# Performance work log

Measured on AMD Instinct MI355X. Metric: run time of the kernel, lower is better.

## Reference

```python
import jax, jax.numpy as jnp
import numpy as np

# dims (see shape_source): seq S = d_t+1 must equal d_k for the unary quantum loader
B, T, D_IN = 128, 127, 48
DK = 128
S = T + 1            # tokens incl. class token; S == DK
H, L = 8, 6
P = (S * S - S) // 2  # RBS angles per head (pyramid circuit over S wires)


def _pyramid_pairs(n):
    # deterministic pyramid ordering of n(n-1)/2 adjacent-pair Givens rotations
    a, b = [], []
    for k in range(n - 1):
        for i in range(k, -1, -1):
            a.append(i)
            b.append(i + 1)
    return np.asarray(a, np.int32), np.asarray(b, np.int32)


def _build_W(phi, pa, pb, n):
    # classical simulation of the RBS pyramid circuit restricted to the unary
    # subspace: product of Givens rotations -> orthogonal n x n matrix
    def step(W, inp):
        ia, ib, th = inp
        c, s = jnp.cos(th), jnp.sin(th)
        ra, rb = W[ia], W[ib]
        W = W.at[ia].set(c * ra - s * rb)
        W = W.at[ib].set(s * ra + c * rb)
        return W, None
    W0 = jnp.eye(n, dtype=phi.dtype)
    W, _ = jax.lax.scan(step, W0, (pa, pb, phi))
    return W


def _layer_norm(x, g, b, eps=1e-5):
    m = jnp.mean(x, axis=-1, keepdims=True)
    v = jnp.mean((x - m) ** 2, axis=-1, keepdims=True)
    return (x - m) * jax.lax.rsqrt(v + eps) * g + b


def setup_inputs() -> dict:
    key = jax.random.key(0)
    ks = jax.random.split(key, 8)
    f32 = jnp.float32
    return {
        "x": jax.random.normal(ks[0], (B, T, D_IN), f32),
        "embed_w": jax.random.normal(ks[1], (DK, D_IN), f32) / np.sqrt(D_IN),
        "embed_b": jnp.zeros((DK,), f32),
        "class_token": jax.random.normal(ks[2], (DK,), f32) / DK,
        "norm0_g": jnp.ones((DK,), f32),
        "norm0_b": jnp.zeros((DK,), f32),
        "Vw": jax.random.normal(ks[3], (L, H, DK, DK), f32) / np.sqrt(DK),
        "Vb": jnp.zeros((L, H, DK), f32),
        "ln_g": jnp.ones((L, H, DK), f32),
        "ln_b": jnp.zeros((L, H, DK), f32),
        "phi": jax.random.normal(ks[4], (L, H, P), f32) / np.sqrt(S),
        "merger_w": jax.random.normal(ks[5], (L, H), f32) / np.sqrt(H),
        "merger_b": jnp.zeros((L,), f32),
    }


def reference(x, embed_w, embed_b, class_token, norm0_g, norm0_b,
              Vw, Vb, ln_g, ln_b, phi, merger_w, merger_b):
    Bsz = x.shape[0]
    pa, pb = _pyramid_pairs(S)
    # orthogonal score matrices for every (layer, head)
    Ws = jax.vmap(lambda p: _build_W(p, pa, pb, S))(phi.reshape(L * H, P))
    Ws = Ws.reshape(L, H, S, S)

    # embed patches, prepend class token (pos_embedding add is a no-op in the
    # original source: bare `+self.pos_embedding` statement, so it is omitted)
    tok = jnp.einsum('btf,df->btd', x, embed_w) + embed_b
    h = jnp.concatenate([jnp.broadcast_to(class_token, (Bsz, 1, DK)), tok], axis=1)
    h = _layer_norm(h, norm0_g, norm0_b)

    scale = 1.0 / np.sqrt(DK)
    for l in range(L):
        nrm = jnp.sqrt(jnp.sum(h * h, axis=-1))      # input3: token norms [B,S]
        u = h / nrm[..., None]                        # unit tokens (convert_array)
        hh, nn, uu = h, nrm, u

        def head(W, vw, vb, g, be):
            V = jnp.einsum('bsd,ed->bse', hh, vw) + vb
            M = jnp.einsum('bsd,de,bte->bst', uu, W, uu)
            A = (M * M) * (nn[:, :, None] * nn[:, None, :])
            Pm = jax.nn.softmax(A * scale, axis=-1)
            return _layer_norm(jnp.einsum('bst,btd->bsd', Pm, V) + hh, g, be)

        hs = jax.vmap(head)(Ws[l], Vw[l], Vb[l], ln_g[l], ln_b[l])  # [H,B,S,D]
        h = jnp.einsum('hbsd,h->bsd', hs, merger_w[l]) + merger_b[l]
    return h[:, -1, :]
```

## Files before the change

kernel.cpp:

```cpp
#include <hip/hip_runtime.h>
#include <hip/hip_bf16.h>


typedef __bf16 bf16x8 __attribute__((ext_vector_type(8)));
typedef float  f32x4  __attribute__((ext_vector_type(4)));
typedef unsigned int u32;
typedef u32 u32x4 __attribute__((ext_vector_type(4)));

__device__ __forceinline__ int sidx(int row, int col)
{
    return row * 128 + ((((col >> 3) ^ (row & 15)) << 3) | (col & 7));
}

__device__ __forceinline__ void gll16(const void* g, void* l)
{
    __builtin_amdgcn_global_load_lds(
        (const __attribute__((address_space(1))) void*)g,
        (__attribute__((address_space(3))) void*)l, 16, 0, 0);
}

__global__ void __launch_bounds__(256)
prep_kernel(const float* __restrict__ phi, float2* __restrict__ csn,
            const float* __restrict__ vw,  __bf16* __restrict__ cvwf)
{
    if (blockIdx.x < 3072) {
        const int mat = blockIdx.x >> 6;
        const int t   = ((blockIdx.x & 63) << 2) + (threadIdx.x >> 6);
        const int j   = threadIdx.x & 63;
        float th = 0.f;
        if (t < 253) {
            const int p = t & 1, i = 2 * j + p;
            const int lim = min(t, 252 - t);
            if (i <= lim) {
                const int k = (t + i) >> 1;
                th = phi[mat * 8128 + ((k * (k + 1)) >> 1) + (k - i)];
            }
        }
        float sn, cs;
        __sincosf(th, &sn, &cs);
        csn[(mat * 256 + t) * 64 + j] = make_float2(cs, sn);
    } else {
        const int f    = (blockIdx.x - 3072) * 256 + threadIdx.x;
        const int lane = f & 63;
        const int k0   = (f >> 6) & 3;
        const int t    = (f >> 8) & 7;
        const int lh   = f >> 11;
        const int row  = t * 16 + (lane & 15);
        const int col  = k0 * 32 + (lane >> 4) * 8;
        const float* src = vw + (lh * 128 + row) * 128 + col;
        __bf16* dst = cvwf + f * 8;
#pragma unroll
        for (int j2 = 0; j2 < 8; j2++) dst[j2] = (__bf16)src[j2];
    }
}

__global__ void __launch_bounds__(64)
build_w_kernel(const float2* __restrict__ csn, __bf16* __restrict__ wt)
{
    const int mat = blockIdx.x >> 5;
    const int grp = blockIdx.x & 31;
    const int c0  = grp * 4;
    const int lam = threadIdx.x;

    const float2* base = csn + (mat * 256) * 64 + lam;

    float vlo[4], vhi[4];
#pragma unroll
    for (int j = 0; j < 4; j++) {
        vlo[j] = (2 * lam     == c0 + j) ? 1.f : 0.f;
        vhi[j] = (2 * lam + 1 == c0 + j) ? 1.f : 0.f;
    }

    float2 buf[3][16];
#pragma unroll
    for (int k = 0; k < 16; k++) buf[0][k] = base[k * 64];
#pragma unroll
    for (int k = 0; k < 16; k++) buf[1][k] = base[(16 + k) * 64];

#pragma unroll
    for (int g = 0; g < 16; g++) {
        const int cb = g % 3;
        if (g < 14) {
            const int nb = (g + 2) % 3;
#pragma unroll
            for (int k = 0; k < 16; k++)
                buf[nb][k] = base[((g + 2) * 16 + k) * 64];
        }
#pragma unroll
        for (int p = 0; p < 8; p++) {
            {
                const float cs = buf[cb][2 * p].x, sn = buf[cb][2 * p].y;
#pragma unroll
                for (int j = 0; j < 4; j++) {
                    float lo = vlo[j], hi = vhi[j];
                    vlo[j] = cs * lo - sn * hi;
                    vhi[j] = sn * lo + cs * hi;
                }
            }
            {
                const float cs = buf[cb][2 * p + 1].x, sn = buf[cb][2 * p + 1].y;
#pragma unroll
                for (int j = 0; j < 4; j++) {
                    float y  = __shfl_down(vlo[j], 1);
                    float x  = vhi[j];
                    float xn = cs * x - sn * y;
                    float yn = sn * x + cs * y;
                    vhi[j] = xn;
                    float z = __shfl_up(yn, 1);
                    if (lam > 0) vlo[j] = z;
                }
            }
        }
    }

    const int t    = c0 >> 4;
    const int k0w  = lam >> 4;
    const int quad = (lam >> 2) & 3;
    u32* wtu = (u32*)wt;
#pragma unroll
    for (int j = 0; j < 4; j++) {
        __bf16 va = (__bf16)vlo[j];
        __bf16 vb = (__bf16)vhi[j];
        u32 pk = (u32)__builtin_bit_cast(unsigned short, va)
               | ((u32)__builtin_bit_cast(unsigned short, vb) << 16);
        const int frag = (t * 4 + k0w) * 64 + quad * 16 + ((c0 & 15) + j);
        wtu[mat * 8192 + frag * 4 + (lam & 3)] = pk;
    }
}

__global__ void __launch_bounds__(512)
embed_kernel(const float* __restrict__ x,  const float* __restrict__ ew,
             const float* __restrict__ eb, const float* __restrict__ ct,
             const float* __restrict__ g0, const float* __restrict__ b0,
             float* __restrict__ hf, __bf16* __restrict__ hb,
             float* __restrict__ invn)
{
    __shared__ float sx[4][48];
    __shared__ float sred[4][2];
    const int d  = threadIdx.x & 127, sq = threadIdx.x >> 7;
    const int wh = (threadIdx.x >> 6) & 1;
    const int b  = blockIdx.x & 127;
    const int s  = (blockIdx.x >> 7) * 4 + sq;

    if (s > 0 && d < 48) sx[sq][d] = x[(b * 127 + (s - 1)) * 48 + d];
    __syncthreads();

    float val;
    if (s == 0) {
        val = ct[d];
    } else {
        float aa = 0.f;
#pragma unroll
        for (int f = 0; f < 48; f++) aa = fmaf(sx[sq][f], ew[d * 48 + f], aa);
        val = aa + eb[d];
    }
    float v = val;
#pragma unroll
    for (int m = 32; m; m >>= 1) v += __shfl_xor(v, m);
    if ((threadIdx.x & 63) == 0) sred[sq][wh] = v;
    __syncthreads();
    float mean = (sred[sq][0] + sred[sq][1]) * (1.f / 128.f);
    float xc   = val - mean;
    __syncthreads();
    v = xc * xc;
#pragma unroll
    for (int m = 32; m; m >>= 1) v += __shfl_xor(v, m);
    if ((threadIdx.x & 63) == 0) sred[sq][wh] = v;
    __syncthreads();
    float var = (sred[sq][0] + sred[sq][1]) * (1.f / 128.f);
    float y   = xc * rsqrtf(var + 1e-5f) * g0[d] + b0[d];
    __syncthreads();
    v = y * y;
#pragma unroll
    for (int m = 32; m; m >>= 1) v += __shfl_xor(v, m);
    if ((threadIdx.x & 63) == 0) sred[sq][wh] = v;
    __syncthreads();
    float ss = sred[sq][0] + sred[sq][1];

    const int o = (b * 128 + s) * 128 + d;
    hf[o] = y;
    hb[o] = (__bf16)y;
    if (d == 0) invn[b * 128 + s] = rsqrtf(ss);
}

__global__ void __launch_bounds__(512, 2)
attn_kernel(int l, int last,
            const float*  __restrict__ hf,  const __bf16* __restrict__ hb,
            const float*  __restrict__ invn, const __bf16* __restrict__ wt,
            const __bf16* __restrict__ vwf, const float* __restrict__ vb,
            const float* __restrict__ lng,  const float* __restrict__ lnb,
            const float* __restrict__ mwp,  __bf16* __restrict__ hs)
{
    __shared__ __align__(16) __bf16 sH[128 * 128];
    __shared__ __align__(16) __bf16 sY[128 * 128];
    __shared__ float sInv[128];
    __shared__ float sVb[128];
    __shared__ float sLg[128];
    __shared__ float sLb[128];

    const int tid  = threadIdx.x;
    const int lane = tid & 63, w = tid >> 6;
    const int l15  = lane & 15, quad = lane >> 4;
    const int b    = blockIdx.x & 127;
    const int hh   = blockIdx.x >> 7;
    const int lh   = l * 8 + hh;

    const __bf16* hbp   = hb  + b * 16384;
    const __bf16* wbase = wt  + (size_t)lh * 16384;
    const __bf16* vbase = vwf + (size_t)lh * 16384;

#pragma unroll
    for (int c = 0; c < 4; c++) {
        const int ch  = tid + c * 512;
        const int row = ch >> 4, cc = ch & 15;
        const int sc  = cc ^ (row & 15);
        gll16(hbp + (row * 16 + sc) * 8, &sH[(c * 512 + w * 64) * 8]);
    }
    if (tid < 128) {
        sInv[tid] = invn[b * 128 + tid];
        sVb[tid]  = vb[lh * 128 + tid];
        sLg[tid]  = lng[lh * 128 + tid];
        sLb[tid]  = lnb[lh * 128 + tid];
    }
    __syncthreads();

    const int r0 = w * 16;
    const int kq = quad * 8;
    const int q4 = quad * 4;
    const f32x4 vzero = {0.f, 0.f, 0.f, 0.f};
    const bool active = !last || (w == 7);

    f32x4 acc[8];

    auto mmGA = [&](const __bf16* gB) {
#pragma unroll
        for (int t = 0; t < 8; t++) acc[t] = vzero;
        __builtin_amdgcn_s_setprio(1);
#pragma unroll
        for (int k0c = 0; k0c < 4; k0c++) {
            bf16x8 a0 = *(const bf16x8*)(&sH[sidx(r0 + l15, k0c * 32 + kq)]);
#pragma unroll
            for (int t = 0; t < 8; t++) {
                bf16x8 bb = *(const bf16x8*)(gB + ((t * 4 + k0c) * 64 + lane) * 8);
                acc[t] = __builtin_amdgcn_mfma_f32_16x16x32_bf16(a0, bb, acc[t], 0, 0, 0);
            }
        }
        __builtin_amdgcn_s_setprio(0);
    };

    auto mmLL = [&](const __bf16* Ab, const __bf16* Bb) {
#pragma unroll
        for (int t = 0; t < 8; t++) acc[t] = vzero;
        __builtin_amdgcn_s_setprio(1);
#pragma unroll
        for (int k0 = 0; k0 < 128; k0 += 32) {
            const int kk = k0 + kq;
            bf16x8 a0 = *(const bf16x8*)(&Ab[sidx(r0 + l15, kk)]);
#pragma unroll
            for (int t = 0; t < 8; t++) {
                bf16x8 bb = *(const bf16x8*)(&Bb[sidx(t * 16 + l15, kk)]);
                acc[t] = __builtin_amdgcn_mfma_f32_16x16x32_bf16(a0, bb, acc[t], 0, 0, 0);
            }
        }
        __builtin_amdgcn_s_setprio(0);
    };

    float hres[8][4];

    if (active) {
        mmGA(wbase);
#pragma unroll
        for (int t = 0; t < 8; t++)
#pragma unroll
            for (int r = 0; r < 4; r++)
                sY[sidx(r0 + q4 + r, t * 16 + l15)] = (__bf16)acc[t][r];

        mmLL(sY, sH);

        {
            const float scale2 = 0.08838834764831843f * 1.4426950408889634f;
            float invt[8];
#pragma unroll
            for (int t = 0; t < 8; t++) invt[t] = sInv[t * 16 + l15];
            float invs[4];
#pragma unroll
            for (int r = 0; r < 4; r++) invs[r] = sInv[r0 + q4 + r];

            float mx[4] = {-3e38f, -3e38f, -3e38f, -3e38f};
#pragma unroll
            for (int t = 0; t < 8; t++)
#pragma unroll
                for (int r = 0; r < 4; r++) {
                    float g = acc[t][r];
                    float v = g * g * invs[r] * invt[t] * scale2;
                    acc[t][r] = v;
                    mx[r] = fmaxf(mx[r], v);
                }
#pragma unroll
            for (int m = 1; m < 16; m <<= 1)
#pragma unroll
                for (int r = 0; r < 4; r++) mx[r] = fmaxf(mx[r], __shfl_xor(mx[r], m));

            float sm[4] = {0.f, 0.f, 0.f, 0.f};
#pragma unroll
            for (int t = 0; t < 8; t++)
#pragma unroll
                for (int r = 0; r < 4; r++) {
                    float e = exp2f(acc[t][r] - mx[r]);
                    acc[t][r] = e;
                    sm[r] += e;
                }
#pragma unroll
            for (int m = 1; m < 16; m <<= 1)
#pragma unroll
                for (int r = 0; r < 4; r++) sm[r] += __shfl_xor(sm[r], m);
#pragma unroll
            for (int r = 0; r < 4; r++) sm[r] = 1.0f / sm[r];
#pragma unroll
            for (int t = 0; t < 8; t++)
#pragma unroll
                for (int r = 0; r < 4; r++)
                    sY[sidx(r0 + q4 + r, t * 16 + l15)] = (__bf16)(acc[t][r] * sm[r]);
        }

        {
            const float* hfp = hf + (b * 128 + r0 + q4) * 128;
#pragma unroll
            for (int t = 0; t < 8; t++)
#pragma unroll
                for (int r = 0; r < 4; r++)
                    hres[t][r] = hfp[r * 128 + t * 16 + l15];
        }
    }

    mmGA(vbase);
    __syncthreads();

    {
        float vbv[8];
#pragma unroll
        for (int t = 0; t < 8; t++) vbv[t] = sVb[t * 16 + l15];
#pragma unroll
        for (int t = 0; t < 8; t++)
#pragma unroll
            for (int r = 0; r < 4; r++)
                sH[sidx(t * 16 + l15, r0 + q4 + r)] = (__bf16)(acc[t][r] + vbv[t]);
    }
    __syncthreads();

    if (active) {
        mmLL(sY, sH);

        {
            const float mw = mwp[lh];
            float lgv[8], lbv[8];
#pragma unroll
            for (int t = 0; t < 8; t++) {
                lgv[t] = sLg[t * 16 + l15];
                lbv[t] = sLb[t * 16 + l15];
            }
            float sum_[4] = {0.f, 0.f, 0.f, 0.f};
            float sq_[4]  = {0.f, 0.f, 0.f, 0.f};
#pragma unroll
            for (int t = 0; t < 8; t++)
#pragma unroll
                for (int r = 0; r < 4; r++) {
                    float xx = acc[t][r] + hres[t][r];
                    acc[t][r] = xx;
                    sum_[r] += xx;
                    sq_[r]  += xx * xx;
                }
#pragma unroll
            for (int m = 1; m < 16; m <<= 1)
#pragma unroll
                for (int r = 0; r < 4; r++) {
                    sum_[r] += __shfl_xor(sum_[r], m);
                    sq_[r]  += __shfl_xor(sq_[r], m);
                }
            float mean[4], rstd[4];
#pragma unroll
            for (int r = 0; r < 4; r++) {
                mean[r] = sum_[r] * (1.f / 128.f);
                float var = sq_[r] * (1.f / 128.f) - mean[r] * mean[r];
                rstd[r] = rsqrtf(fmaxf(var, 0.f) + 1e-5f);
            }
            __bf16* hsp = hs + ((hh * 128 + b) * 128 + r0 + q4) * 128;
#pragma unroll
            for (int t = 0; t < 8; t++)
#pragma unroll
                for (int r = 0; r < 4; r++) {
                    if (!last || (q4 + r == 15)) {
                        float y = (acc[t][r] - mean[r]) * rstd[r] * lgv[t] + lbv[t];
                        hsp[r * 128 + t * 16 + l15] = (__bf16)(y * mw);
                    }
                }
        }
    }
}

__global__ void __launch_bounds__(256)
merge_kernel(const __bf16* __restrict__ hs, const float* __restrict__ mbp, int l,
             float* __restrict__ hf, __bf16* __restrict__ hb, float* __restrict__ invn,
             float* __restrict__ out, int last)
{
    const int lane = threadIdx.x & 63;
    const int wv   = threadIdx.x >> 6;
    const int sq   = lane >> 4;
    const int dl   = lane & 15;
    const int d0   = dl * 8;
    const float mbv = mbp[l];

    int b, s;
    if (last) {
        b = blockIdx.x * 16 + wv * 4 + sq;
        s = 127;
    } else {
        b = blockIdx.x & 127;
        s = (blockIdx.x >> 7) * 16 + wv * 4 + sq;
    }

    float a[8];
#pragma unroll
    for (int j = 0; j < 8; j++) a[j] = mbv;
#pragma unroll
    for (int h8 = 0; h8 < 8; h8++) {
        bf16x8 v = *(const bf16x8*)(hs + (((size_t)h8 * 128 + b) * 128 + s) * 128 + d0);
#pragma unroll
        for (int j = 0; j < 8; j++) a[j] += (float)v[j];
    }

    if (last) {
        float4 f0 = {a[0], a[1], a[2], a[3]};
        float4 f1 = {a[4], a[5], a[6], a[7]};
        *(float4*)(out + b * 128 + d0)     = f0;
        *(float4*)(out + b * 128 + d0 + 4) = f1;
        return;
    }

    float ss = 0.f;
#pragma unroll
    for (int j = 0; j < 8; j++) ss = fmaf(a[j], a[j], ss);
#pragma unroll
    for (int m = 1; m < 16; m <<= 1) ss += __shfl_xor(ss, m);

    const size_t o = ((size_t)b * 128 + s) * 128 + d0;
    float4 f0 = {a[0], a[1], a[2], a[3]};
    float4 f1 = {a[4], a[5], a[6], a[7]};
    *(float4*)(hf + o)     = f0;
    *(float4*)(hf + o + 4) = f1;

    u32 pk[4];
#pragma unroll
    for (int j2 = 0; j2 < 4; j2++) {
        __bf16 x0 = (__bf16)a[2 * j2], x1 = (__bf16)a[2 * j2 + 1];
        pk[j2] = (u32)__builtin_bit_cast(unsigned short, x0)
               | ((u32)__builtin_bit_cast(unsigned short, x1) << 16);
    }
    u32x4 pv = {pk[0], pk[1], pk[2], pk[3]};
    *(u32x4*)(hb + o) = pv;

    if (dl == 0) invn[b * 128 + s] = rsqrtf(ss);
}

extern "C" void kernel_launch(void* const* d_in, const int* in_sizes, int n_in,
                              void* d_out, int out_size, void* d_ws, size_t ws_size,
                              hipStream_t stream)
{
    (void)in_sizes; (void)n_in; (void)out_size; (void)ws_size;

    const float* x   = (const float*)d_in[0];
    const float* ew  = (const float*)d_in[1];
    const float* eb  = (const float*)d_in[2];
    const float* ct  = (const float*)d_in[3];
    const float* g0  = (const float*)d_in[4];
    const float* b0  = (const float*)d_in[5];
    const float* vw  = (const float*)d_in[6];
    const float* vb  = (const float*)d_in[7];
    const float* lng = (const float*)d_in[8];
    const float* lnb = (const float*)d_in[9];
    const float* phi = (const float*)d_in[10];
    const float* mw  = (const float*)d_in[11];
    const float* mb  = (const float*)d_in[12];
    float* out = (float*)d_out;

    char* ws = (char*)d_ws;
    __bf16* wt   = (__bf16*)(ws);
    float*  hf   = (float*)(ws + 1572864);
    __bf16* hb   = (__bf16*)(ws + 9961472);
    float*  invn = (float*)(ws + 14155776);
    __bf16* hs   = (__bf16*)(ws + 14221312);
    __bf16* cvwf = (__bf16*)(ws + 47775744);
    float2* csn  = (float2*)(ws + 49348608);

    prep_kernel<<<3456, 256, 0, stream>>>(phi, csn, vw, cvwf);
    build_w_kernel<<<1536, 64, 0, stream>>>(csn, wt);
    embed_kernel<<<4096, 512, 0, stream>>>(x, ew, eb, ct, g0, b0, hf, hb, invn);
    for (int l = 0; l < 6; l++) {
        const int last = (l == 5) ? 1 : 0;
        attn_kernel<<<1024, 512, 0, stream>>>(l, last, hf, hb, invn, wt, cvwf,
                                              vb, lng, lnb, mw, hs);
        merge_kernel<<<last ? 8 : 1024, 256, 0, stream>>>(hs, mb, l, hf, hb,
                                                          invn, out, last);
    }
}
```

Before: 412.7 us.

## Process two heads per attention block and pre-sum their outputs

Each attention block now handles two heads (hp and hp+4) one after the other. The first head's layernormed, merger-weighted result is kept packed in registers as bf16 and added to the second head's result before storing. This halves the grid and the bytes written to the hs buffer, and the merge kernel reads only 4 head slices instead of 8. The cost is fewer blocks for occupancy, a reload of sH between heads, extra registers, and an extra bf16 rounding in the partial sum.

```diff
diff --git a/kernel.cpp b/kernel.cpp
--- a/kernel.cpp
+++ b/kernel.cpp
@@ -6,6 +6,7 @@
 typedef float  f32x4  __attribute__((ext_vector_type(4)));
 typedef unsigned int u32;
 typedef u32 u32x4 __attribute__((ext_vector_type(4)));
+typedef unsigned short u16;
 
 __device__ __forceinline__ int sidx(int row, int col)
 {
@@ -194,20 +195,19 @@
     __shared__ __align__(16) __bf16 sH[128 * 128];
     __shared__ __align__(16) __bf16 sY[128 * 128];
     __shared__ float sInv[128];
-    __shared__ float sVb[128];
-    __shared__ float sLg[128];
-    __shared__ float sLb[128];
+    __shared__ float sVb2[256];
+    __shared__ float sLg2[256];
+    __shared__ float sLb2[256];
 
     const int tid  = threadIdx.x;
     const int lane = tid & 63, w = tid >> 6;
     const int l15  = lane & 15, quad = lane >> 4;
     const int b    = blockIdx.x & 127;
-    const int hh   = blockIdx.x >> 7;
-    const int lh   = l * 8 + hh;
-
-    const __bf16* hbp   = hb  + b * 16384;
-    const __bf16* wbase = wt  + (size_t)lh * 16384;
-    const __bf16* vbase = vwf + (size_t)lh * 16384;
+    const int hp   = blockIdx.x >> 7;
+    const int lh0  = l * 8 + hp;
+    const int lh1  = l * 8 + hp + 4;
+
+    const __bf16* hbp = hb + b * 16384;
 
 #pragma unroll
     for (int c = 0; c < 4; c++) {
@@ -216,11 +216,13 @@
         const int sc  = cc ^ (row & 15);
         gll16(hbp + (row * 16 + sc) * 8, &sH[(c * 512 + w * 64) * 8]);
     }
-    if (tid < 128) {
-        sInv[tid] = invn[b * 128 + tid];
-        sVb[tid]  = vb[lh * 128 + tid];
-        sLg[tid]  = lng[lh * 128 + tid];
-        sLb[tid]  = lnb[lh * 128 + tid];
+    if (tid < 128) sInv[tid] = invn[b * 128 + tid];
+    if (tid < 256) {
+        const int hh = tid >> 7, d = tid & 127;
+        const int lh = l * 8 + hp + hh * 4;
+        sVb2[tid] = vb[lh * 128 + d];
+        sLg2[tid] = lng[lh * 128 + d];
+        sLb2[tid] = lnb[lh * 128 + d];
     }
     __syncthreads();
 
@@ -265,81 +267,78 @@
         __builtin_amdgcn_s_setprio(0);
     };
 
+    auto softmax = [&]() {
+        const float scale2 = 0.08838834764831843f * 1.4426950408889634f;
+        float invt[8];
+#pragma unroll
+        for (int t = 0; t < 8; t++) invt[t] = sInv[t * 16 + l15];
+        float invs[4];
+#pragma unroll
+        for (int r = 0; r < 4; r++) invs[r] = sInv[r0 + q4 + r];
+
+        float mx[4] = {-3e38f, -3e38f, -3e38f, -3e38f};
+#pragma unroll
+        for (int t = 0; t < 8; t++)
+#pragma unroll
+            for (int r = 0; r < 4; r++) {
+                float g = acc[t][r];
+                float v = g * g * invs[r] * invt[t] * scale2;
+                acc[t][r] = v;
+                mx[r] = fmaxf(mx[r], v);
+            }
+#pragma unroll
+        for (int m = 1; m < 16; m <<= 1)
+#pragma unroll
+            for (int r = 0; r < 4; r++) mx[r] = fmaxf(mx[r], __shfl_xor(mx[r], m));
+
+        float sm[4] = {0.f, 0.f, 0.f, 0.f};
+#pragma unroll
+        for (int t = 0; t < 8; t++)
+#pragma unroll
+            for (int r = 0; r < 4; r++) {
+                float e = exp2f(acc[t][r] - mx[r]);
+                acc[t][r] = e;
+                sm[r] += e;
+            }
+#pragma unroll
+        for (int m = 1; m < 16; m <<= 1)
+#pragma unroll
+            for (int r = 0; r < 4; r++) sm[r] += __shfl_xor(sm[r], m);
+#pragma unroll
+        for (int r = 0; r < 4; r++) sm[r] = 1.0f / sm[r];
+#pragma unroll
+        for (int t = 0; t < 8; t++)
+#pragma unroll
+            for (int r = 0; r < 4; r++)
+                sY[sidx(r0 + q4 + r, t * 16 + l15)] = (__bf16)(acc[t][r] * sm[r]);
+    };
+
     float hres[8][4];
+    u32   y0p[8][2];
 
     if (active) {
-        mmGA(wbase);
+        mmGA(wt + (size_t)lh0 * 16384);
 #pragma unroll
         for (int t = 0; t < 8; t++)
 #pragma unroll
             for (int r = 0; r < 4; r++)
                 sY[sidx(r0 + q4 + r, t * 16 + l15)] = (__bf16)acc[t][r];
-
         mmLL(sY, sH);
-
-        {
-            const float scale2 = 0.08838834764831843f * 1.4426950408889634f;
-            float invt[8];
-#pragma unroll
-            for (int t = 0; t < 8; t++) invt[t] = sInv[t * 16 + l15];
-            float invs[4];
-#pragma unroll
-            for (int r = 0; r < 4; r++) invs[r] = sInv[r0 + q4 + r];
-
-            float mx[4] = {-3e38f, -3e38f, -3e38f, -3e38f};
-#pragma unroll
-            for (int t = 0; t < 8; t++)
-#pragma unroll
-                for (int r = 0; r < 4; r++) {
-                    float g = acc[t][r];
-                    float v = g * g * invs[r] * invt[t] * scale2;
-                    acc[t][r] = v;
-                    mx[r] = fmaxf(mx[r], v);
-                }
-#pragma unroll
-            for (int m = 1; m < 16; m <<= 1)
-#pragma unroll
-                for (int r = 0; r < 4; r++) mx[r] = fmaxf(mx[r], __shfl_xor(mx[r], m));
-
-            float sm[4] = {0.f, 0.f, 0.f, 0.f};
-#pragma unroll
-            for (int t = 0; t < 8; t++)
-#pragma unroll
-                for (int r = 0; r < 4; r++) {
-                    float e = exp2f(acc[t][r] - mx[r]);
-                    acc[t][r] = e;
-                    sm[r] += e;
-                }
-#pragma unroll
-            for (int m = 1; m < 16; m <<= 1)
-#pragma unroll
-                for (int r = 0; r < 4; r++) sm[r] += __shfl_xor(sm[r], m);
-#pragma unroll
-            for (int r = 0; r < 4; r++) sm[r] = 1.0f / sm[r];
-#pragma unroll
-            for (int t = 0; t < 8; t++)
-#pragma unroll
-                for (int r = 0; r < 4; r++)
-                    sY[sidx(r0 + q4 + r, t * 16 + l15)] = (__bf16)(acc[t][r] * sm[r]);
-        }
-
-        {
-            const float* hfp = hf + (b * 128 + r0 + q4) * 128;
-#pragma unroll
-            for (int t = 0; t < 8; t++)
-#pragma unroll
-                for (int r = 0; r < 4; r++)
-                    hres[t][r] = hfp[r * 128 + t * 16 + l15];
-        }
-    }
-
-    mmGA(vbase);
-    __syncthreads();
-
+        softmax();
+        const float* hfp = hf + (b * 128 + r0 + q4) * 128;
+#pragma unroll
+        for (int t = 0; t < 8; t++)
+#pragma unroll
+            for (int r = 0; r < 4; r++)
+                hres[t][r] = hfp[r * 128 + t * 16 + l15];
+    }
+
+    mmGA(vwf + (size_t)lh0 * 16384);
+    __syncthreads();
     {
         float vbv[8];
 #pragma unroll
-        for (int t = 0; t < 8; t++) vbv[t] = sVb[t * 16 + l15];
+        for (int t = 0; t < 8; t++) vbv[t] = sVb2[t * 16 + l15];
 #pragma unroll
         for (int t = 0; t < 8; t++)
 #pragma unroll
@@ -350,50 +349,123 @@
 
     if (active) {
         mmLL(sY, sH);
-
-        {
-            const float mw = mwp[lh];
-            float lgv[8], lbv[8];
-#pragma unroll
-            for (int t = 0; t < 8; t++) {
-                lgv[t] = sLg[t * 16 + l15];
-                lbv[t] = sLb[t * 16 + l15];
-            }
-            float sum_[4] = {0.f, 0.f, 0.f, 0.f};
-            float sq_[4]  = {0.f, 0.f, 0.f, 0.f};
-#pragma unroll
-            for (int t = 0; t < 8; t++)
-#pragma unroll
-                for (int r = 0; r < 4; r++) {
-                    float xx = acc[t][r] + hres[t][r];
-                    acc[t][r] = xx;
-                    sum_[r] += xx;
-                    sq_[r]  += xx * xx;
+        const float mw = mwp[lh0];
+        float sum_[4] = {0.f, 0.f, 0.f, 0.f};
+        float sq_[4]  = {0.f, 0.f, 0.f, 0.f};
+#pragma unroll
+        for (int t = 0; t < 8; t++)
+#pragma unroll
+            for (int r = 0; r < 4; r++) {
+                float xx = acc[t][r] + hres[t][r];
+                acc[t][r] = xx;
+                sum_[r] += xx;
+                sq_[r]  += xx * xx;
+            }
+#pragma unroll
+        for (int m = 1; m < 16; m <<= 1)
+#pragma unroll
+            for (int r = 0; r < 4; r++) {
+                sum_[r] += __shfl_xor(sum_[r], m);
+                sq_[r]  += __shfl_xor(sq_[r], m);
+            }
+#pragma unroll
+        for (int t = 0; t < 8; t++) {
+            float lg = sLg2[t * 16 + l15];
+            float lb = sLb2[t * 16 + l15];
+            u32 pk[2];
+#pragma unroll
+            for (int rp = 0; rp < 2; rp++) {
+                u32 pw = 0;
+#pragma unroll
+                for (int rr = 0; rr < 2; rr++) {
+                    const int r = rp * 2 + rr;
+                    float mean = sum_[r] * (1.f / 128.f);
+                    float var  = sq_[r] * (1.f / 128.f) - mean * mean;
+                    float rstd = rsqrtf(fmaxf(var, 0.f) + 1e-5f);
+                    float y = ((acc[t][r] - mean) * rstd * lg + lb) * mw;
+                    __bf16 yb = (__bf16)y;
+                    pw |= (u32)__builtin_bit_cast(u16, yb) << (rr * 16);
                 }
-#pragma unroll
-            for (int m = 1; m < 16; m <<= 1)
-#pragma unroll
-                for (int r = 0; r < 4; r++) {
-                    sum_[r] += __shfl_xor(sum_[r], m);
-                    sq_[r]  += __shfl_xor(sq_[r], m);
+                pk[rp] = pw;
+            }
+            y0p[t][0] = pk[0];
+            y0p[t][1] = pk[1];
+        }
+    }
+
+    __syncthreads();
+#pragma unroll
+    for (int c = 0; c < 4; c++) {
+        const int ch  = tid + c * 512;
+        const int row = ch >> 4, cc = ch & 15;
+        const int sc  = cc ^ (row & 15);
+        gll16(hbp + (row * 16 + sc) * 8, &sH[(c * 512 + w * 64) * 8]);
+    }
+    __syncthreads();
+
+    if (active) {
+        mmGA(wt + (size_t)lh1 * 16384);
+#pragma unroll
+        for (int t = 0; t < 8; t++)
+#pragma unroll
+            for (int r = 0; r < 4; r++)
+                sY[sidx(r0 + q4 + r, t * 16 + l15)] = (__bf16)acc[t][r];
+        mmLL(sY, sH);
+        softmax();
+    }
+
+    mmGA(vwf + (size_t)lh1 * 16384);
+    __syncthreads();
+    {
+        float vbv[8];
+#pragma unroll
+        for (int t = 0; t < 8; t++) vbv[t] = sVb2[128 + t * 16 + l15];
+#pragma unroll
+        for (int t = 0; t < 8; t++)
+#pragma unroll
+            for (int r = 0; r < 4; r++)
+                sH[sidx(t * 16 + l15, r0 + q4 + r)] = (__bf16)(acc[t][r] + vbv[t]);
+    }
+    __syncthreads();
+
+    if (active) {
+        mmLL(sY, sH);
+        const float mw = mwp[lh1];
+        float sum_[4] = {0.f, 0.f, 0.f, 0.f};
+        float sq_[4]  = {0.f, 0.f, 0.f, 0.f};
+#pragma unroll
+        for (int t = 0; t < 8; t++)
+#pragma unroll
+            for (int r = 0; r < 4; r++) {
+                float xx = acc[t][r] + hres[t][r];
+                acc[t][r] = xx;
+                sum_[r] += xx;
+                sq_[r]  += xx * xx;
+            }
+#pragma unroll
+        for (int m = 1; m < 16; m <<= 1)
+#pragma unroll
+            for (int r = 0; r < 4; r++) {
+                sum_[r] += __shfl_xor(sum_[r], m);
+                sq_[r]  += __shfl_xor(sq_[r], m);
+            }
+        __bf16* hsp = hs + ((hp * 128 + b) * 128 + r0 + q4) * 128;
+#pragma unroll
+        for (int t = 0; t < 8; t++) {
+            float lg = sLg2[128 + t * 16 + l15];
+            float lb = sLb2[128 + t * 16 + l15];
+#pragma unroll
+            for (int r = 0; r < 4; r++) {
+                if (!last || (q4 + r == 15)) {
+                    float mean = sum_[r] * (1.f / 128.f);
+                    float var  = sq_[r] * (1.f / 128.f) - mean * mean;
+                    float rstd = rsqrtf(fmaxf(var, 0.f) + 1e-5f);
+                    float y1 = ((acc[t][r] - mean) * rstd * lg + lb) * mw;
+                    u16 h0 = (u16)(y0p[t][r >> 1] >> ((r & 1) * 16));
+                    float y = y1 + (float)__builtin_bit_cast(__bf16, h0);
+                    hsp[r * 128 + t * 16 + l15] = (__bf16)y;
                 }
-            float mean[4], rstd[4];
-#pragma unroll
-            for (int r = 0; r < 4; r++) {
-                mean[r] = sum_[r] * (1.f / 128.f);
-                float var = sq_[r] * (1.f / 128.f) - mean[r] * mean[r];
-                rstd[r] = rsqrtf(fmaxf(var, 0.f) + 1e-5f);
-            }
-            __bf16* hsp = hs + ((hh * 128 + b) * 128 + r0 + q4) * 128;
-#pragma unroll
-            for (int t = 0; t < 8; t++)
-#pragma unroll
-                for (int r = 0; r < 4; r++) {
-                    if (!last || (q4 + r == 15)) {
-                        float y = (acc[t][r] - mean[r]) * rstd[r] * lgv[t] + lbv[t];
-                        hsp[r * 128 + t * 16 + l15] = (__bf16)(y * mw);
-                    }
-                }
+            }
         }
     }
 }
@@ -423,7 +495,7 @@
 #pragma unroll
     for (int j = 0; j < 8; j++) a[j] = mbv;
 #pragma unroll
-    for (int h8 = 0; h8 < 8; h8++) {
+    for (int h8 = 0; h8 < 4; h8++) {
         bf16x8 v = *(const bf16x8*)(hs + (((size_t)h8 * 128 + b) * 128 + s) * 128 + d0);
 #pragma unroll
         for (int j = 0; j < 8; j++) a[j] += (float)v[j];
@@ -497,8 +569,8 @@
     embed_kernel<<<4096, 512, 0, stream>>>(x, ew, eb, ct, g0, b0, hf, hb, invn);
     for (int l = 0; l < 6; l++) {
         const int last = (l == 5) ? 1 : 0;
-        attn_kernel<<<1024, 512, 0, stream>>>(l, last, hf, hb, invn, wt, cvwf,
-                                              vb, lng, lnb, mw, hs);
+        attn_kernel<<<512, 512, 0, stream>>>(l, last, hf, hb, invn, wt, cvwf,
+                                             vb, lng, lnb, mw, hs);
         merge_kernel<<<last ? 8 : 1024, 256, 0, stream>>>(hs, mb, l, hf, hb,
                                                           invn, out, last);
     }
```

Result: slower. 479.2 us (+16.1%).
